# Optimization experiments

Measured on AMD Instinct MI355X. Metric: run time of the kernel, lower is better.

## Reference

```python
import jax, jax.numpy as jnp
import numpy as np

B, N, D = 4, 256, 256
NEG = -1e9


def setup_inputs() -> dict:
    key = jax.random.key(0)
    k = jax.random.split(key, 5)
    scale1 = 1.0 / np.sqrt(4 * D)
    scale2 = 1.0 / np.sqrt(D)
    return {
        "shared": jax.random.normal(k[0], (B, N, D), dtype=jnp.float32),
        "W1": jax.random.uniform(k[1], (4 * D, D), jnp.float32, -scale1, scale1),
        "b1": jax.random.uniform(k[2], (D,), jnp.float32, -scale1, scale1),
        "W2": jax.random.uniform(k[3], (D, 1), jnp.float32, -scale2, scale2),
        "b2": jax.random.uniform(k[4], (1,), jnp.float32, -scale2, scale2),
    }


def reference(shared, W1, b1, W2, b2):
    # Linear on concat([src, tgt, |src-tgt|, src*tgt]) == sum of per-block matmuls.
    Wa, Wb, Wc, Wd = W1[:D], W1[D:2 * D], W1[2 * D:3 * D], W1[3 * D:]
    src_t = jnp.einsum('bid,dh->bih', shared, Wa)        # [B,N,D]
    tgt_t = jnp.einsum('bjd,dh->bjh', shared, Wb)        # [B,N,D]
    diff = jnp.abs(shared[:, :, None, :] - shared[:, None, :, :])  # [B,N,N,D]
    prod = shared[:, :, None, :] * shared[:, None, :, :]           # [B,N,N,D]
    h = (src_t[:, :, None, :] + tgt_t[:, None, :, :]
         + jnp.einsum('bijd,dh->bijh', diff, Wc)
         + jnp.einsum('bijd,dh->bijh', prod, Wd) + b1)   # [B,N,N,D]
    h = jax.nn.silu(h)
    scores = jnp.einsum('bijh,h->bij', h, W2[:, 0]) + b2[0]  # [B,N,N]
    eye = jnp.eye(N, dtype=bool)[None]
    scores = jnp.where(eye, NEG, scores)
    return jax.nn.softmax(scores, axis=-1)
```

## Files before the change

kernel.cpp:

```cpp
#include <hip/hip_runtime.h>

#define BB 4
#define NN 256
#define DD 256
#define HH 256
#define NEGV -1.0e9f

typedef _Float16 half8 __attribute__((ext_vector_type(8)));
typedef __fp16   fp16x2 __attribute__((ext_vector_type(2)));
typedef float floatx4 __attribute__((ext_vector_type(4)));

__global__ __launch_bounds__(256) void prep_split(const float* __restrict__ X,
                                                  const float* __restrict__ W1,
                                                  float* __restrict__ S,
                                                  float* __restrict__ T,
                                                  _Float16* __restrict__ Wst) {
  const int g  = blockIdx.x;
  const int kk = blockIdx.y;
  const int h  = threadIdx.x;

  if (kk == 0 && g < 256) {
    const float wcv = W1[(size_t)(2 * DD + g) * HH + h];
    const float wdv = W1[(size_t)(3 * DD + g) * HH + h];
    const int ks = g >> 4;
    const int dd = g & 15;
    const int q  = dd >> 2;
    const int e  = (dd & 3) * 2;
    const int hgrp = h >> 4;
    const int ccw  = h & 15;
    _Float16* p = Wst + ((size_t)((ks * 16 + hgrp) * 4 + q) * 16 + ccw) * 8 + e;
    p[0] = (_Float16)wcv;
    p[1] = (_Float16)wdv;
  }

  const int row0 = g * 2;
  const int dbase = kk * 128;
  __shared__ float xr[2][128];
  if (h < 128) xr[0][h] = X[(size_t)row0 * DD + dbase + h];
  else         xr[1][h - 128] = X[(size_t)(row0 + 1) * DD + dbase + (h - 128)];
  __syncthreads();

  const float* __restrict__ Wa = W1 + (size_t)dbase * HH;
  const float* __restrict__ Wb = W1 + (size_t)(DD + dbase) * HH;
  float sa0 = 0.f, sa1 = 0.f, sb0 = 0.f, sb1 = 0.f;
#pragma unroll 8
  for (int d = 0; d < 128; ++d) {
    const float wa = Wa[(size_t)d * HH + h];
    const float wb = Wb[(size_t)d * HH + h];
    sa0 = fmaf(xr[0][d], wa, sa0);  sb0 = fmaf(xr[0][d], wb, sb0);
    sa1 = fmaf(xr[1][d], wa, sa1);  sb1 = fmaf(xr[1][d], wb, sb1);
  }
  atomicAdd(&S[(size_t)(row0 + 0) * HH + h], sa0);
  atomicAdd(&T[(size_t)(row0 + 0) * HH + h], sb0);
  atomicAdd(&S[(size_t)(row0 + 1) * HH + h], sa1);
  atomicAdd(&T[(size_t)(row0 + 1) * HH + h], sb1);
}

__device__ __forceinline__ half8 make_afrag(const float4 xi, const float4 xj) {
  fp16x2 p0 = __builtin_amdgcn_cvt_pkrtz(__builtin_fabsf(xi.x - xj.x), xi.x * xj.x);
  fp16x2 p1 = __builtin_amdgcn_cvt_pkrtz(__builtin_fabsf(xi.y - xj.y), xi.y * xj.y);
  fp16x2 p2 = __builtin_amdgcn_cvt_pkrtz(__builtin_fabsf(xi.z - xj.z), xi.z * xj.z);
  fp16x2 p3 = __builtin_amdgcn_cvt_pkrtz(__builtin_fabsf(xi.w - xj.w), xi.w * xj.w);
  uint4 u;
  u.x = __builtin_bit_cast(unsigned int, p0);
  u.y = __builtin_bit_cast(unsigned int, p1);
  u.z = __builtin_bit_cast(unsigned int, p2);
  u.w = __builtin_bit_cast(unsigned int, p3);
  return __builtin_bit_cast(half8, u);
}

#define MFMA16(af, bf, acc) acc = __builtin_amdgcn_mfma_f32_16x16x32_f16(af, bf, acc, 0, 0, 0)

__global__ __launch_bounds__(256, 2) void score_mfma(
    const float* __restrict__ X,  const float* __restrict__ b1,
    const float* __restrict__ W2, const float* __restrict__ b2,
    const float* __restrict__ S,  const float* __restrict__ T,
    const _Float16* __restrict__ Wst, float* __restrict__ Sc) {

  const int beta = blockIdx.x;
  const int b    = blockIdx.y;
  int i, qt;
  if (beta < 256)      { i = beta >> 2;                    qt = beta & 3; }
  else if (beta < 448) { const int g = beta - 256; const int d3 = g / 3;
                         i = 64 + d3;                      qt = 1 + (g - 3 * d3); }
  else if (beta < 576) { const int g = beta - 448;
                         i = 128 + (g >> 1);               qt = 2 + (g & 1); }
  else                 { i = 192 + (beta - 576);           qt = 3; }
  const int bi    = b * NN + i;
  const int jbase = qt * 64;
  const int isUp  = qt > (i >> 6);

  const int t     = threadIdx.x;
  const int lane  = t & 63;
  const int hg    = t >> 6;
  const int q     = lane >> 4;
  const int cc    = lane & 15;

  __shared__ __align__(16) float    xi_s[DD];
  __shared__ __align__(16) _Float16 Af[16384];
  __shared__ float pre_s[HH];
  __shared__ float pre2_s[HH];
  __shared__ float w2_s[HH];
  __shared__ float sc_s[4][64];

  xi_s[t]   = X[(size_t)bi * DD + t];
  pre_s[t]  = S[(size_t)bi * HH + t] + b1[t];
  pre2_s[t] = T[(size_t)bi * HH + t] + b1[t];
  w2_s[t]   = W2[t];

  const float* __restrict__ Tb = T + (size_t)b * NN * HH;
  const float* __restrict__ Sb = S + (size_t)b * NN * HH;

  const int jloc = t & 63;
  const int jg   = jloc >> 4;
  const int ccw  = jloc & 15;
  const float* __restrict__ xjrow = X + (size_t)(b * NN + jbase + jloc) * DD;

  const char* __restrict__ bsrc = (const char*)Wst + hg * 4096 + (size_t)lane * 16;

  floatx4 a00 = (floatx4)0.f, a01 = (floatx4)0.f, a02 = (floatx4)0.f, a03 = (floatx4)0.f;
  floatx4 a10 = (floatx4)0.f, a11 = (floatx4)0.f, a12 = (floatx4)0.f, a13 = (floatx4)0.f;
  floatx4 a20 = (floatx4)0.f, a21 = (floatx4)0.f, a22 = (floatx4)0.f, a23 = (floatx4)0.f;
  floatx4 a30 = (floatx4)0.f, a31 = (floatx4)0.f, a32 = (floatx4)0.f, a33 = (floatx4)0.f;

#pragma unroll 1
  for (int half = 0; half < 2; ++half) {
    __syncthreads();

#pragma unroll
    for (int idx = 0; idx < 8; ++idx) {
      const int ksq = (t >> 6) * 8 + idx;
      const int d0  = (half * 32 + ksq) * 4;
      const int ksl = ksq >> 2;
      const int qw  = ksq & 3;
      const float4 xi4 = *(const float4*)&xi_s[d0];
      const float4 xj4 = *(const float4*)(xjrow + d0);
      *(half8*)&Af[(ksl * 16 + jg * 4 + qw) * 128 + ccw * 8] = make_afrag(xi4, xj4);
    }
    __syncthreads();

    const char* bk0 = bsrc + (half * 8) * 16384;
    half8 nb0 = *(const half8*)(bk0);
    half8 nb1 = *(const half8*)(bk0 + 1024);
    half8 nb2 = *(const half8*)(bk0 + 2048);
    half8 nb3 = *(const half8*)(bk0 + 3072);
    const _Float16* ap0 = &Af[lane * 8];
    half8 na0 = *(const half8*)(ap0);
    half8 na1 = *(const half8*)(ap0 + 512);
    half8 na2 = *(const half8*)(ap0 + 1024);
    half8 na3 = *(const half8*)(ap0 + 1536);

#pragma unroll
    for (int ksl = 0; ksl < 8; ++ksl) {
      const half8 cb0 = nb0, cb1 = nb1, cb2 = nb2, cb3 = nb3;
      const half8 ca0 = na0, ca1 = na1, ca2 = na2, ca3 = na3;
      if (ksl < 7) {
        const char* bk = bsrc + (half * 8 + ksl + 1) * 16384;
        nb0 = *(const half8*)(bk);
        nb1 = *(const half8*)(bk + 1024);
        nb2 = *(const half8*)(bk + 2048);
        nb3 = *(const half8*)(bk + 3072);
        const _Float16* ap = &Af[(ksl + 1) * 2048 + lane * 8];
        na0 = *(const half8*)(ap);
        na1 = *(const half8*)(ap + 512);
        na2 = *(const half8*)(ap + 1024);
        na3 = *(const half8*)(ap + 1536);
      }
      MFMA16(ca0, cb0, a00); MFMA16(ca0, cb1, a01); MFMA16(ca0, cb2, a02); MFMA16(ca0, cb3, a03);
      MFMA16(ca1, cb0, a10); MFMA16(ca1, cb1, a11); MFMA16(ca1, cb2, a12); MFMA16(ca1, cb3, a13);
      MFMA16(ca2, cb0, a20); MFMA16(ca2, cb1, a21); MFMA16(ca2, cb2, a22); MFMA16(ca2, cb3, a23);
      MFMA16(ca3, cb0, a30); MFMA16(ca3, cb1, a31); MFMA16(ca3, cb2, a32); MFMA16(ca3, cb3, a33);
    }
  }

  float p00, p01, p02, p03, p10, p11, p12, p13;
  float p20, p21, p22, p23, p30, p31, p32, p33;
  p00=p01=p02=p03=p10=p11=p12=p13=0.f;
  p20=p21=p22=p23=p30=p31=p32=p33=0.f;

#define SILU_DOT(A, r, VROW, PREV, P) { \
    const float tv = VROW[(size_t)(jbase + jj16 + q * 4 + r) * HH + h]; \
    const float hv = A[r] + PREV + tv; \
    const float sv = hv * __builtin_amdgcn_rcpf(1.f + __expf(-hv)); \
    P = fmaf(sv, w2v, P); }

#define EPI_HH(hh, A0, A1, A2, A3, VROW, PRE) { \
    const int h = hg * 64 + hh * 16 + cc; \
    const float w2v = w2_s[h]; \
    const float pv  = PRE[h]; \
    { const int jj16 = 0;  SILU_DOT(A0, 0, VROW, pv, p00) SILU_DOT(A0, 1, VROW, pv, p01) \
                           SILU_DOT(A0, 2, VROW, pv, p02) SILU_DOT(A0, 3, VROW, pv, p03) } \
    { const int jj16 = 16; SILU_DOT(A1, 0, VROW, pv, p10) SILU_DOT(A1, 1, VROW, pv, p11) \
                           SILU_DOT(A1, 2, VROW, pv, p12) SILU_DOT(A1, 3, VROW, pv, p13) } \
    { const int jj16 = 32; SILU_DOT(A2, 0, VROW, pv, p20) SILU_DOT(A2, 1, VROW, pv, p21) \
                           SILU_DOT(A2, 2, VROW, pv, p22) SILU_DOT(A2, 3, VROW, pv, p23) } \
    { const int jj16 = 48; SILU_DOT(A3, 0, VROW, pv, p30) SILU_DOT(A3, 1, VROW, pv, p31) \
                           SILU_DOT(A3, 2, VROW, pv, p32) SILU_DOT(A3, 3, VROW, pv, p33) } }

#define REDW(P, jj, r) { \
    float v = P; \
    v += __shfl_xor(v, 1); v += __shfl_xor(v, 2); \
    v += __shfl_xor(v, 4); v += __shfl_xor(v, 8); \
    if (cc == 0) sc_s[hg][jj * 16 + q * 4 + r] = v; }

#define REDW_ALL \
  REDW(p00, 0, 0) REDW(p01, 0, 1) REDW(p02, 0, 2) REDW(p03, 0, 3) \
  REDW(p10, 1, 0) REDW(p11, 1, 1) REDW(p12, 1, 2) REDW(p13, 1, 3) \
  REDW(p20, 2, 0) REDW(p21, 2, 1) REDW(p22, 2, 2) REDW(p23, 2, 3) \
  REDW(p30, 3, 0) REDW(p31, 3, 1) REDW(p32, 3, 2) REDW(p33, 3, 3)

  EPI_HH(0, a00, a10, a20, a30, Tb, pre_s)
  EPI_HH(1, a01, a11, a21, a31, Tb, pre_s)
  EPI_HH(2, a02, a12, a22, a32, Tb, pre_s)
  EPI_HH(3, a03, a13, a23, a33, Tb, pre_s)
  REDW_ALL
  __syncthreads();

  if (t < 64) {
    float s = sc_s[0][t] + sc_s[1][t] + sc_s[2][t] + sc_s[3][t] + b2[0];
    const int jg2 = jbase + t;
    if (jg2 == i) s = NEGV;
    Sc[(size_t)bi * NN + jg2] = s;
  }

  if (isUp) {
    __syncthreads();
    p00=p01=p02=p03=p10=p11=p12=p13=0.f;
    p20=p21=p22=p23=p30=p31=p32=p33=0.f;
    EPI_HH(0, a00, a10, a20, a30, Sb, pre2_s)
    EPI_HH(1, a01, a11, a21, a31, Sb, pre2_s)
    EPI_HH(2, a02, a12, a22, a32, Sb, pre2_s)
    EPI_HH(3, a03, a13, a23, a33, Sb, pre2_s)
    REDW_ALL
    __syncthreads();
    if (t < 64) {
      const float s = sc_s[0][t] + sc_s[1][t] + sc_s[2][t] + sc_s[3][t] + b2[0];
      Sc[(size_t)(b * NN + jbase + t) * NN + i] = s;
    }
  }
}

__global__ __launch_bounds__(256) void softmax_kernel(const float* __restrict__ Sc,
                                                      float* __restrict__ out) {
  const int bi = blockIdx.x;
  const int t  = threadIdx.x;
  __shared__ float red[NN];
  const float s = Sc[(size_t)bi * NN + t];
  red[t] = s;
  __syncthreads();
  for (int k = 128; k > 0; k >>= 1) {
    if (t < k) red[t] = fmaxf(red[t], red[t + k]);
    __syncthreads();
  }
  const float m = red[0];
  __syncthreads();
  const float e = __expf(s - m);
  red[t] = e;
  __syncthreads();
  for (int k = 128; k > 0; k >>= 1) {
    if (t < k) red[t] += red[t + k];
    __syncthreads();
  }
  out[(size_t)bi * NN + t] = e / red[0];
}

extern "C" void kernel_launch(void* const* d_in, const int* in_sizes, int n_in,
                              void* d_out, int out_size, void* d_ws, size_t ws_size,
                              hipStream_t stream) {
  const float* X  = (const float*)d_in[0];
  const float* W1 = (const float*)d_in[1];
  const float* b1 = (const float*)d_in[2];
  const float* W2 = (const float*)d_in[3];
  const float* b2 = (const float*)d_in[4];
  float* out = (float*)d_out;

  float*     Sws = (float*)d_ws;
  float*     Tws = Sws + (size_t)BB * NN * HH;
  _Float16*  Wst = (_Float16*)(Tws + (size_t)BB * NN * HH);
  float*     Scw = (float*)(Wst + (size_t)16 * HH * 32);

  hipMemsetAsync(Sws, 0, (size_t)2 * BB * NN * HH * sizeof(float), stream);

  prep_split<<<dim3(512, 2), 256, 0, stream>>>(X, W1, Sws, Tws, Wst);
  score_mfma<<<dim3(640, BB), 256, 0, stream>>>(X, b1, W2, b2, Sws, Tws, Wst, Scw);
  softmax_kernel<<<BB * NN, 256, 0, stream>>>(Scw, out);
}
```

Measured before the change: 171.7 us.

## Split prep reduction four ways, raise score occupancy, warp-per-row softmax

The prep kernel now splits the d-reduction into four 64-wide chunks instead of two 128-wide ones. This doubles the number of blocks, at the cost of more atomic adds. The score kernel's launch bounds ask for 4 blocks per SM instead of 2, which may force register spills. The softmax is rewritten so each 64-lane wavefront handles one row with float4 loads and shuffle reductions, replacing the shared-memory tree with its many barriers.

```diff
diff --git a/kernel.cpp b/kernel.cpp
--- a/kernel.cpp
+++ b/kernel.cpp
@@ -34,17 +34,17 @@
   }
 
   const int row0 = g * 2;
-  const int dbase = kk * 128;
-  __shared__ float xr[2][128];
-  if (h < 128) xr[0][h] = X[(size_t)row0 * DD + dbase + h];
-  else         xr[1][h - 128] = X[(size_t)(row0 + 1) * DD + dbase + (h - 128)];
+  const int dbase = kk * 64;
+  __shared__ float xr[2][64];
+  if (h < 64)       xr[0][h]      = X[(size_t)row0 * DD + dbase + h];
+  else if (h < 128) xr[1][h - 64] = X[(size_t)(row0 + 1) * DD + dbase + (h - 64)];
   __syncthreads();
 
   const float* __restrict__ Wa = W1 + (size_t)dbase * HH;
   const float* __restrict__ Wb = W1 + (size_t)(DD + dbase) * HH;
   float sa0 = 0.f, sa1 = 0.f, sb0 = 0.f, sb1 = 0.f;
 #pragma unroll 8
-  for (int d = 0; d < 128; ++d) {
+  for (int d = 0; d < 64; ++d) {
     const float wa = Wa[(size_t)d * HH + h];
     const float wb = Wb[(size_t)d * HH + h];
     sa0 = fmaf(xr[0][d], wa, sa0);  sb0 = fmaf(xr[0][d], wb, sb0);
@@ -71,7 +71,7 @@
 
 #define MFMA16(af, bf, acc) acc = __builtin_amdgcn_mfma_f32_16x16x32_f16(af, bf, acc, 0, 0, 0)
 
-__global__ __launch_bounds__(256, 2) void score_mfma(
+__global__ __launch_bounds__(256, 4) void score_mfma(
     const float* __restrict__ X,  const float* __restrict__ b1,
     const float* __restrict__ W2, const float* __restrict__ b2,
     const float* __restrict__ S,  const float* __restrict__ T,
@@ -242,26 +242,23 @@
 
 __global__ __launch_bounds__(256) void softmax_kernel(const float* __restrict__ Sc,
                                                       float* __restrict__ out) {
-  const int bi = blockIdx.x;
-  const int t  = threadIdx.x;
-  __shared__ float red[NN];
-  const float s = Sc[(size_t)bi * NN + t];
-  red[t] = s;
-  __syncthreads();
-  for (int k = 128; k > 0; k >>= 1) {
-    if (t < k) red[t] = fmaxf(red[t], red[t + k]);
-    __syncthreads();
-  }
-  const float m = red[0];
-  __syncthreads();
-  const float e = __expf(s - m);
-  red[t] = e;
-  __syncthreads();
-  for (int k = 128; k > 0; k >>= 1) {
-    if (t < k) red[t] += red[t + k];
-    __syncthreads();
-  }
-  out[(size_t)bi * NN + t] = e / red[0];
+  const int w    = threadIdx.x >> 6;
+  const int lane = threadIdx.x & 63;
+  const int bi   = blockIdx.x * 4 + w;
+  const float4 v = *(const float4*)&Sc[(size_t)bi * NN + lane * 4];
+  float m = fmaxf(fmaxf(v.x, v.y), fmaxf(v.z, v.w));
+  m = fmaxf(m, __shfl_xor(m, 1));  m = fmaxf(m, __shfl_xor(m, 2));
+  m = fmaxf(m, __shfl_xor(m, 4));  m = fmaxf(m, __shfl_xor(m, 8));
+  m = fmaxf(m, __shfl_xor(m, 16)); m = fmaxf(m, __shfl_xor(m, 32));
+  const float e0 = __expf(v.x - m), e1 = __expf(v.y - m);
+  const float e2 = __expf(v.z - m), e3 = __expf(v.w - m);
+  float sum = (e0 + e1) + (e2 + e3);
+  sum += __shfl_xor(sum, 1);  sum += __shfl_xor(sum, 2);
+  sum += __shfl_xor(sum, 4);  sum += __shfl_xor(sum, 8);
+  sum += __shfl_xor(sum, 16); sum += __shfl_xor(sum, 32);
+  const float r = 1.f / sum;
+  float4 o; o.x = e0 * r; o.y = e1 * r; o.z = e2 * r; o.w = e3 * r;
+  *(float4*)&out[(size_t)bi * NN + lane * 4] = o;
 }
 
 extern "C" void kernel_launch(void* const* d_in, const int* in_sizes, int n_in,
@@ -281,7 +278,7 @@
 
   hipMemsetAsync(Sws, 0, (size_t)2 * BB * NN * HH * sizeof(float), stream);
 
-  prep_split<<<dim3(512, 2), 256, 0, stream>>>(X, W1, Sws, Tws, Wst);
+  prep_split<<<dim3(512, 4), 256, 0, stream>>>(X, W1, Sws, Tws, Wst);
   score_mfma<<<dim3(640, BB), 256, 0, stream>>>(X, b1, W2, b2, Sws, Tws, Wst, Scw);
-  softmax_kernel<<<BB * NN, 256, 0, stream>>>(Scw, out);
-}
+  softmax_kernel<<<BB * NN / 4, 256, 0, stream>>>(Scw, out);
+}
```

Result: slower. 268.1 us (+56.1%).
